# Kernel tuning notes

Measured on AMD Instinct MI355X. Metric: run time of the kernel, lower is better.

## Reference

```python
import jax, jax.numpy as jnp
import numpy as np

EMB = 1024
HEADS = 16
HEAD_SIZE = EMB // HEADS  # 64
B, T = 2, 2048


def setup_inputs() -> dict:
    key = jax.random.key(0)
    k1, k2, k3 = jax.random.split(key, 3)
    x = jax.random.normal(k1, (B, T, EMB), dtype=jnp.float32)
    # scale weights like typical init to keep logits sane
    w_qkv = jax.random.normal(k2, (EMB, 3 * EMB), dtype=jnp.float32) * (EMB ** -0.5)
    w_proj = jax.random.normal(k3, (EMB, EMB), dtype=jnp.float32) * (EMB ** -0.5)
    b_proj = jnp.zeros((EMB,), dtype=jnp.float32)
    return {"x": x, "w_qkv": w_qkv, "w_proj": w_proj, "b_proj": b_proj}


def reference(x, w_qkv, w_proj, b_proj):
    Bb, Tt, C = x.shape
    qkv = x @ w_qkv  # [B,T,3C]
    q, k, v = jnp.split(qkv, 3, axis=-1)
    # [B,H,T,hs]
    q = q.reshape(Bb, Tt, HEADS, HEAD_SIZE).transpose(0, 2, 1, 3)
    k = k.reshape(Bb, Tt, HEADS, HEAD_SIZE).transpose(0, 2, 1, 3)
    v = v.reshape(Bb, Tt, HEADS, HEAD_SIZE).transpose(0, 2, 1, 3)
    scale = HEAD_SIZE ** -0.5
    wei = jnp.einsum('bhqd,bhkd->bhqk', q, k) * scale  # [B,H,T,T]
    causal = jnp.tril(jnp.ones((Tt, Tt), dtype=bool))
    wei = jnp.where(causal, wei, -jnp.inf)
    wei = jax.nn.softmax(wei, axis=-1)
    out = jnp.einsum('bhqk,bhkd->bhqd', wei, v)  # [B,H,T,hs]
    out = out.transpose(0, 2, 1, 3).reshape(Bb, Tt, C)
    out = out @ w_proj + b_proj
    return out
```

## Files before the change

kernel.cpp:

```cpp
#include <hip/hip_runtime.h>
#include <hip/hip_bf16.h>

typedef __attribute__((ext_vector_type(8))) short short8;
typedef __attribute__((ext_vector_type(4))) float floatx4;

#define MFMA16(a, b, c) __builtin_amdgcn_mfma_f32_16x16x32_bf16((a), (b), (c), 0, 0, 0)
#define GLOBAL_AS __attribute__((address_space(1)))
#define LDS_AS __attribute__((address_space(3)))

__device__ __forceinline__ unsigned short f2bf(float x) {
  union { float f; unsigned u; } v; v.f = x;
  unsigned r = v.u + 0x7FFFu + ((v.u >> 16) & 1u);
  return (unsigned short)(r >> 16);
}

__device__ __forceinline__ short8 ld8(const unsigned short* p) {
  return *reinterpret_cast<const short8*>(p);
}

__device__ __forceinline__ void async_cp16(const unsigned short* g, unsigned short* l) {
  __builtin_amdgcn_global_load_lds((const GLOBAL_AS void*)g, (LDS_AS void*)l, 16, 0, 0);
}

__global__ void k_f32_to_bf16(const float* __restrict__ in,
                              unsigned short* __restrict__ out, int n4) {
  int i = blockIdx.x * blockDim.x + threadIdx.x;
  if (i >= n4) return;
  float4 f = reinterpret_cast<const float4*>(in)[i];
  union { unsigned short u[4]; unsigned long long v; } o;
  o.u[0] = f2bf(f.x); o.u[1] = f2bf(f.y); o.u[2] = f2bf(f.z); o.u[3] = f2bf(f.w);
  reinterpret_cast<unsigned long long*>(out)[i] = o.v;
}

__global__ void k_transpose_bf16(const float* __restrict__ in,
                                 unsigned short* __restrict__ out, int R, int C) {
  __shared__ float tile[64][65];
  int c0 = blockIdx.x * 64, r0 = blockIdx.y * 64;
  int tx = threadIdx.x, ty = threadIdx.y;
  for (int i = ty; i < 64; i += 4)
    tile[i][tx] = in[(size_t)(r0 + i) * C + c0 + tx];
  __syncthreads();
  for (int i = ty; i < 64; i += 4)
    out[(size_t)(c0 + i) * R + r0 + tx] = f2bf(tile[tx][i]);
}

__global__ void k_vtrans(const unsigned short* __restrict__ qkvb,
                         unsigned short* __restrict__ vT) {
  const int T = 2048, LD = 3072;
  __shared__ unsigned short tile[64][72];
  int bh = blockIdx.y, b = bh >> 4, h = bh & 15;
  int t0 = blockIdx.x * 64;
  int tx = threadIdx.x, ty = threadIdx.y;
  const unsigned short* src = qkvb + (size_t)b * T * LD + 2048 + h * 64;
  for (int i = ty; i < 64; i += 4)
    tile[i][tx] = src[(size_t)(t0 + i) * LD + tx];
  __syncthreads();
  unsigned short* dst = vT + (size_t)bh * 64 * T;
  for (int i = ty; i < 64; i += 4)
    dst[(size_t)i * T + t0 + tx] = tile[tx][i];
}

template <int OUT_BF16, int HAS_BIAS>
__global__ __launch_bounds__(256) void k_gemm_bt(
    const unsigned short* __restrict__ A, const unsigned short* __restrict__ Bt,
    void* __restrict__ Cout, const float* __restrict__ bias, int M, int N, int K) {
  __shared__ unsigned short As[128][64];
  __shared__ unsigned short Bs[128][64];
  int tid = threadIdx.x;
  int w = tid >> 6, lane = tid & 63, quad = lane >> 4, l16 = lane & 15;
  int wy = w >> 1, wx = w & 1;
  int rowB = blockIdx.y * 128, colB = blockIdx.x * 128;
  int srcRow = lane >> 3;
  int srcCol = (((lane & 7) ^ (srcRow & 7)) << 3);

  floatx4 acc[4][4];
  floatx4 zero4 = {0.f, 0.f, 0.f, 0.f};
#pragma unroll
  for (int mi = 0; mi < 4; ++mi)
#pragma unroll
    for (int ni = 0; ni < 4; ++ni) acc[mi][ni] = zero4;

  for (int kt = 0; kt < K; kt += 64) {
    __syncthreads();
#pragma unroll
    for (int i = 0; i < 4; ++i) {
      int r0 = w * 32 + i * 8;
      async_cp16(&A[(size_t)(rowB + r0 + srcRow) * K + kt + srcCol], &As[r0][0]);
      async_cp16(&Bt[(size_t)(colB + r0 + srcRow) * K + kt + srcCol], &Bs[r0][0]);
    }
    __syncthreads();
#pragma unroll
    for (int kh = 0; kh < 2; ++kh) {
      short8 af[4], bf_[4];
#pragma unroll
      for (int mi = 0; mi < 4; ++mi)
        af[mi] = ld8(&As[wy * 64 + mi * 16 + l16][((kh * 4 + quad) ^ (l16 & 7)) << 3]);
#pragma unroll
      for (int ni = 0; ni < 4; ++ni)
        bf_[ni] = ld8(&Bs[wx * 64 + ni * 16 + l16][((kh * 4 + quad) ^ (l16 & 7)) << 3]);
#pragma unroll
      for (int mi = 0; mi < 4; ++mi)
#pragma unroll
        for (int ni = 0; ni < 4; ++ni)
          acc[mi][ni] = MFMA16(af[mi], bf_[ni], acc[mi][ni]);
    }
  }

#pragma unroll
  for (int mi = 0; mi < 4; ++mi) {
    int row = rowB + wy * 64 + mi * 16 + quad * 4;
#pragma unroll
    for (int ni = 0; ni < 4; ++ni) {
      int col = colB + wx * 64 + ni * 16 + l16;
      float bv = HAS_BIAS ? bias[col] : 0.f;
#pragma unroll
      for (int r = 0; r < 4; ++r) {
        float val = acc[mi][ni][r] + bv;
        if (OUT_BF16)
          ((unsigned short*)Cout)[(size_t)(row + r) * N + col] = f2bf(val);
        else
          ((float*)Cout)[(size_t)(row + r) * N + col] = val;
      }
    }
  }
}

__global__ __launch_bounds__(256) void k_attn(
    const unsigned short* __restrict__ qkv, const unsigned short* __restrict__ vT,
    unsigned short* __restrict__ attn_out) {
  const int T = 2048, LD = 3072;
  __shared__ unsigned short Kt[64][72];
  __shared__ unsigned short Vt[64][72];
  __shared__ unsigned short Pt[4][2][16][72];

  int bh = blockIdx.y, b = bh >> 4, h = bh & 15;
  int ip = blockIdx.x;
  int tid = threadIdx.x, w = tid >> 6, lane = tid & 63;
  int quad = lane >> 4, l16 = lane & 15;

  const unsigned short* Qp = qkv + (size_t)b * T * LD + h * 64;
  const unsigned short* Kp = Qp + 1024;
  const unsigned short* Vp = vT + (size_t)bh * 64 * T;

  const int q0s[2] = {ip * 64, (31 - ip) * 64};
  const int lastkt[2] = {ip, 31 - ip};
  int nt = 32 - ip;

  short8 aq[2][2];
#pragma unroll
  for (int m = 0; m < 2; ++m) {
    const unsigned short* qrow = Qp + (size_t)(q0s[m] + w * 16 + l16) * LD + quad * 8;
    aq[m][0] = ld8(qrow);
    aq[m][1] = ld8(qrow + 32);
  }

  short8 ones8;
  {
    unsigned short o = 0x3F80;
#pragma unroll
    for (int j = 0; j < 8; ++j) ones8[j] = (short)o;
  }

  const float cscale = 0.125f * 1.44269504f;
  floatx4 o_acc[2][4], l_acc[2];
  floatx4 zero4 = {0.f, 0.f, 0.f, 0.f};
#pragma unroll
  for (int m = 0; m < 2; ++m) {
    l_acc[m] = zero4;
#pragma unroll
    for (int nd = 0; nd < 4; ++nd) o_acc[m][nd] = zero4;
  }

  int stR = tid >> 3, stC = (tid & 7) << 3;

  short8 kreg[2], vreg[2];
#pragma unroll
  for (int j = 0; j < 2; ++j) {
    int r = stR + j * 32;
    kreg[j] = ld8(&Kp[(size_t)r * LD + stC]);
    vreg[j] = ld8(&Vp[(size_t)r * T + stC]);
  }

  for (int kt = 0; kt < nt; ++kt) {
    __syncthreads();
#pragma unroll
    for (int j = 0; j < 2; ++j) {
      int r = stR + j * 32;
      *reinterpret_cast<short8*>(&Kt[r][stC]) = kreg[j];
      *reinterpret_cast<short8*>(&Vt[r][stC]) = vreg[j];
    }
    __syncthreads();

    if (kt + 1 < nt) {
      int key0n = (kt + 1) * 64;
#pragma unroll
      for (int j = 0; j < 2; ++j) {
        int r = stR + j * 32;
        kreg[j] = ld8(&Kp[(size_t)(key0n + r) * LD + stC]);
        vreg[j] = ld8(&Vp[(size_t)r * T + key0n + stC]);
      }
    }

    int key0 = kt * 64;
    bool act0 = (kt <= lastkt[0]);

    floatx4 st[2][4];
#pragma unroll
    for (int kt4 = 0; kt4 < 4; ++kt4) {
      short8 ak0 = ld8(&Kt[kt4 * 16 + l16][quad * 8]);
      short8 ak1 = ld8(&Kt[kt4 * 16 + l16][32 + quad * 8]);
      st[1][kt4] = MFMA16(ak0, aq[1][0], zero4);
      st[1][kt4] = MFMA16(ak1, aq[1][1], st[1][kt4]);
      if (act0) {
        st[0][kt4] = MFMA16(ak0, aq[0][0], zero4);
        st[0][kt4] = MFMA16(ak1, aq[0][1], st[0][kt4]);
      }
    }

#pragma unroll
    for (int m = 0; m < 2; ++m) {
      if (m == 0 && !act0) continue;
      if (kt == lastkt[m]) {
        int qlane = q0s[m] + w * 16 + l16;
#pragma unroll
        for (int kt4 = 0; kt4 < 4; ++kt4)
#pragma unroll
          for (int r = 0; r < 4; ++r)
            if (key0 + kt4 * 16 + quad * 4 + r > qlane) st[m][kt4][r] = -1e30f;
      }
#pragma unroll
      for (int kt4 = 0; kt4 < 4; ++kt4) {
        unsigned u[4];
#pragma unroll
        for (int r = 0; r < 4; ++r)
          u[r] = __float_as_uint(
              __builtin_amdgcn_exp2f(fmaf(st[m][kt4][r], cscale, -16.f)));
        unsigned lo = __builtin_amdgcn_perm(u[1], u[0], 0x07060302u);
        unsigned hi = __builtin_amdgcn_perm(u[3], u[2], 0x07060302u);
        unsigned long long pv = ((unsigned long long)hi << 32) | lo;
        *reinterpret_cast<unsigned long long*>(
            &Pt[w][m][l16][kt4 * 16 + quad * 4]) = pv;
      }
    }

    short8 pa[2][2];
    pa[1][0] = ld8(&Pt[w][1][l16][quad * 8]);
    pa[1][1] = ld8(&Pt[w][1][l16][32 + quad * 8]);
    if (act0) {
      pa[0][0] = ld8(&Pt[w][0][l16][quad * 8]);
      pa[0][1] = ld8(&Pt[w][0][l16][32 + quad * 8]);
    }
#pragma unroll
    for (int nd = 0; nd < 4; ++nd) {
      short8 bv0 = ld8(&Vt[nd * 16 + l16][quad * 8]);
      short8 bv1 = ld8(&Vt[nd * 16 + l16][32 + quad * 8]);
      o_acc[1][nd] = MFMA16(pa[1][0], bv0, o_acc[1][nd]);
      o_acc[1][nd] = MFMA16(pa[1][1], bv1, o_acc[1][nd]);
      if (act0) {
        o_acc[0][nd] = MFMA16(pa[0][0], bv0, o_acc[0][nd]);
        o_acc[0][nd] = MFMA16(pa[0][1], bv1, o_acc[0][nd]);
      }
    }
    l_acc[1] = MFMA16(pa[1][0], ones8, l_acc[1]);
    l_acc[1] = MFMA16(pa[1][1], ones8, l_acc[1]);
    if (act0) {
      l_acc[0] = MFMA16(pa[0][0], ones8, l_acc[0]);
      l_acc[0] = MFMA16(pa[0][1], ones8, l_acc[0]);
    }
  }

#pragma unroll
  for (int m = 0; m < 2; ++m)
#pragma unroll
    for (int nd = 0; nd < 4; ++nd)
#pragma unroll
      for (int r = 0; r < 4; ++r) {
        int q = q0s[m] + w * 16 + quad * 4 + r;
        int d = nd * 16 + l16;
        attn_out[(size_t)(b * T + q) * 1024 + h * 64 + d] =
            f2bf(o_acc[m][nd][r] / l_acc[m][r]);
      }
}

extern "C" void kernel_launch(void* const* d_in, const int* in_sizes, int n_in,
                              void* d_out, int out_size, void* d_ws, size_t ws_size,
                              hipStream_t stream) {
  const float* x = (const float*)d_in[0];
  const float* w_qkv = (const float*)d_in[1];
  const float* w_proj = (const float*)d_in[2];
  const float* b_proj = (const float*)d_in[3];
  float* out = (float*)d_out;

  char* ws = (char*)d_ws;
  unsigned short* xb     = (unsigned short*)(ws);
  unsigned short* wqkvT  = (unsigned short*)(ws + (size_t)(8  << 20));
  unsigned short* wprojT = (unsigned short*)(ws + (size_t)(14 << 20));
  unsigned short* qkvb   = (unsigned short*)(ws + (size_t)(16 << 20));
  unsigned short* attnb  = (unsigned short*)(ws + (size_t)(40 << 20));
  unsigned short* vTb    = xb;

  k_f32_to_bf16<<<4096, 256, 0, stream>>>(x, xb, (4096 * 1024) / 4);
  dim3 tb(64, 4);
  k_transpose_bf16<<<dim3(3072 / 64, 1024 / 64), tb, 0, stream>>>(w_qkv, wqkvT, 1024, 3072);
  k_transpose_bf16<<<dim3(1024 / 64, 1024 / 64), tb, 0, stream>>>(w_proj, wprojT, 1024, 1024);
  k_gemm_bt<1, 0><<<dim3(3072 / 128, 4096 / 128), 256, 0, stream>>>(
      xb, wqkvT, qkvb, nullptr, 4096, 3072, 1024);
  k_vtrans<<<dim3(2048 / 64, 2 * 16), tb, 0, stream>>>(qkvb, vTb);
  k_attn<<<dim3(16, 2 * 16), 256, 0, stream>>>(qkvb, vTb, attnb);
  k_gemm_bt<0, 1><<<dim3(1024 / 128, 4096 / 128), 256, 0, stream>>>(
      attnb, wprojT, out, b_proj, 4096, 1024, 1024);
}
```

Before: 200.3 us.

## Merge prep kernels, add 128x64 projection GEMM, pad P tile, round P to bf16

Folds the x conversion and both weight transposes into a single prep launch to cut launch overhead. Replaces the projection GEMM with a 128x64-tile kernel so more blocks run at N=1024, with an XOR-swizzled LDS layout and direct global-to-LDS loads. In attention, the P staging row is padded from 72 to 76 to reduce LDS bank conflicts, and P is now rounded to bf16 instead of truncated, which costs one extra add per element. The smaller projection tile gives less data reuse per block, and the new kernel loads into LDS without double buffering.

```diff
diff --git a/kernel.cpp b/kernel.cpp
--- a/kernel.cpp
+++ b/kernel.cpp
@@ -22,21 +22,30 @@
   __builtin_amdgcn_global_load_lds((const GLOBAL_AS void*)g, (LDS_AS void*)l, 16, 0, 0);
 }
 
-__global__ void k_f32_to_bf16(const float* __restrict__ in,
-                              unsigned short* __restrict__ out, int n4) {
-  int i = blockIdx.x * blockDim.x + threadIdx.x;
-  if (i >= n4) return;
-  float4 f = reinterpret_cast<const float4*>(in)[i];
-  union { unsigned short u[4]; unsigned long long v; } o;
-  o.u[0] = f2bf(f.x); o.u[1] = f2bf(f.y); o.u[2] = f2bf(f.z); o.u[3] = f2bf(f.w);
-  reinterpret_cast<unsigned long long*>(out)[i] = o.v;
-}
-
-__global__ void k_transpose_bf16(const float* __restrict__ in,
-                                 unsigned short* __restrict__ out, int R, int C) {
+__global__ __launch_bounds__(256) void k_prep(
+    const float* __restrict__ x, unsigned short* __restrict__ xb,
+    const float* __restrict__ w_qkv, unsigned short* __restrict__ wqkvT,
+    const float* __restrict__ w_proj, unsigned short* __restrict__ wprojT) {
   __shared__ float tile[64][65];
-  int c0 = blockIdx.x * 64, r0 = blockIdx.y * 64;
-  int tx = threadIdx.x, ty = threadIdx.y;
+  int bid = blockIdx.x, tid = threadIdx.x;
+  if (bid < 4096) {
+    int i = bid * 256 + tid;
+    float4 f = reinterpret_cast<const float4*>(x)[i];
+    union { unsigned short u[4]; unsigned long long v; } o;
+    o.u[0] = f2bf(f.x); o.u[1] = f2bf(f.y); o.u[2] = f2bf(f.z); o.u[3] = f2bf(f.w);
+    reinterpret_cast<unsigned long long*>(xb)[i] = o.v;
+    return;
+  }
+  const float* in; unsigned short* out; int R, C, bx, by;
+  if (bid < 4864) {
+    int rel = bid - 4096;
+    in = w_qkv; out = wqkvT; R = 1024; C = 3072; bx = rel % 48; by = rel / 48;
+  } else {
+    int rel = bid - 4864;
+    in = w_proj; out = wprojT; R = 1024; C = 1024; bx = rel % 16; by = rel / 16;
+  }
+  int tx = tid & 63, ty = tid >> 6;
+  int c0 = bx * 64, r0 = by * 64;
   for (int i = ty; i < 64; i += 4)
     tile[i][tx] = in[(size_t)(r0 + i) * C + c0 + tx];
   __syncthreads();
@@ -125,13 +134,75 @@
   }
 }
 
+__global__ __launch_bounds__(256) void k_gemm_proj(
+    const unsigned short* __restrict__ A, const unsigned short* __restrict__ Bt,
+    float* __restrict__ Cout, const float* __restrict__ bias, int M, int N, int K) {
+  __shared__ unsigned short As[128][64];
+  __shared__ unsigned short Bs[64][64];
+  int tid = threadIdx.x;
+  int w = tid >> 6, lane = tid & 63, quad = lane >> 4, l16 = lane & 15;
+  int rowB = blockIdx.y * 128, colB = blockIdx.x * 64;
+  int srcRow = lane >> 3;
+  int srcCol = (((lane & 7) ^ (srcRow & 7)) << 3);
+
+  floatx4 acc[2][4];
+  floatx4 zero4 = {0.f, 0.f, 0.f, 0.f};
+#pragma unroll
+  for (int mi = 0; mi < 2; ++mi)
+#pragma unroll
+    for (int ni = 0; ni < 4; ++ni) acc[mi][ni] = zero4;
+
+  for (int kt = 0; kt < K; kt += 64) {
+    __syncthreads();
+#pragma unroll
+    for (int i = 0; i < 4; ++i) {
+      int r0 = w * 32 + i * 8;
+      async_cp16(&A[(size_t)(rowB + r0 + srcRow) * K + kt + srcCol], &As[r0][0]);
+    }
+#pragma unroll
+    for (int i = 0; i < 2; ++i) {
+      int r0 = w * 16 + i * 8;
+      async_cp16(&Bt[(size_t)(colB + r0 + srcRow) * K + kt + srcCol], &Bs[r0][0]);
+    }
+    __syncthreads();
+#pragma unroll
+    for (int kh = 0; kh < 2; ++kh) {
+      short8 af[2], bf_[4];
+#pragma unroll
+      for (int mi = 0; mi < 2; ++mi)
+        af[mi] = ld8(&As[w * 32 + mi * 16 + l16][((kh * 4 + quad) ^ (l16 & 7)) << 3]);
+#pragma unroll
+      for (int ni = 0; ni < 4; ++ni)
+        bf_[ni] = ld8(&Bs[ni * 16 + l16][((kh * 4 + quad) ^ (l16 & 7)) << 3]);
+#pragma unroll
+      for (int mi = 0; mi < 2; ++mi)
+#pragma unroll
+        for (int ni = 0; ni < 4; ++ni)
+          acc[mi][ni] = MFMA16(af[mi], bf_[ni], acc[mi][ni]);
+    }
+  }
+
+#pragma unroll
+  for (int mi = 0; mi < 2; ++mi) {
+    int row = rowB + w * 32 + mi * 16 + quad * 4;
+#pragma unroll
+    for (int ni = 0; ni < 4; ++ni) {
+      int col = colB + ni * 16 + l16;
+      float bv = bias[col];
+#pragma unroll
+      for (int r = 0; r < 4; ++r)
+        Cout[(size_t)(row + r) * N + col] = acc[mi][ni][r] + bv;
+    }
+  }
+}
+
 __global__ __launch_bounds__(256) void k_attn(
     const unsigned short* __restrict__ qkv, const unsigned short* __restrict__ vT,
     unsigned short* __restrict__ attn_out) {
   const int T = 2048, LD = 3072;
   __shared__ unsigned short Kt[64][72];
   __shared__ unsigned short Vt[64][72];
-  __shared__ unsigned short Pt[4][2][16][72];
+  __shared__ unsigned short Pt[4][2][16][76];
 
   int bh = blockIdx.y, b = bh >> 4, h = bh & 15;
   int ip = blockIdx.x;
@@ -232,9 +303,10 @@
       for (int kt4 = 0; kt4 < 4; ++kt4) {
         unsigned u[4];
 #pragma unroll
-        for (int r = 0; r < 4; ++r)
-          u[r] = __float_as_uint(
-              __builtin_amdgcn_exp2f(fmaf(st[m][kt4][r], cscale, -16.f)));
+        for (int r = 0; r < 4; ++r) {
+          float p = __builtin_amdgcn_exp2f(fmaf(st[m][kt4][r], cscale, -16.f));
+          u[r] = __float_as_uint(p) + 0x8000u;
+        }
         unsigned lo = __builtin_amdgcn_perm(u[1], u[0], 0x07060302u);
         unsigned hi = __builtin_amdgcn_perm(u[3], u[2], 0x07060302u);
         unsigned long long pv = ((unsigned long long)hi << 32) | lo;
@@ -299,14 +371,11 @@
   unsigned short* attnb  = (unsigned short*)(ws + (size_t)(40 << 20));
   unsigned short* vTb    = xb;
 
-  k_f32_to_bf16<<<4096, 256, 0, stream>>>(x, xb, (4096 * 1024) / 4);
-  dim3 tb(64, 4);
-  k_transpose_bf16<<<dim3(3072 / 64, 1024 / 64), tb, 0, stream>>>(w_qkv, wqkvT, 1024, 3072);
-  k_transpose_bf16<<<dim3(1024 / 64, 1024 / 64), tb, 0, stream>>>(w_proj, wprojT, 1024, 1024);
+  k_prep<<<5120, 256, 0, stream>>>(x, xb, w_qkv, wqkvT, w_proj, wprojT);
   k_gemm_bt<1, 0><<<dim3(3072 / 128, 4096 / 128), 256, 0, stream>>>(
       xb, wqkvT, qkvb, nullptr, 4096, 3072, 1024);
-  k_vtrans<<<dim3(2048 / 64, 2 * 16), tb, 0, stream>>>(qkvb, vTb);
+  k_vtrans<<<dim3(2048 / 64, 2 * 16), dim3(64, 4), 0, stream>>>(qkvb, vTb);
   k_attn<<<dim3(16, 2 * 16), 256, 0, stream>>>(qkvb, vTb, attnb);
-  k_gemm_bt<0, 1><<<dim3(1024 / 128, 4096 / 128), 256, 0, stream>>>(
+  k_gemm_proj<<<dim3(1024 / 64, 4096 / 128), 256, 0, stream>>>(
       attnb, wprojT, out, b_proj, 4096, 1024, 1024);
 }
```

New measurement: 202.6 us. About the same (+1.1%).
